# Performance work log

Measured on AMD Instinct MI355X. Metric: run time of the kernel, lower is better.

Reference implementation:

```python
import jax, jax.numpy as jnp
import numpy as np

DIM = 512
N_HEADS = 8
HEAD_DIM = DIM // N_HEADS


def setup_inputs() -> dict:
    key = jax.random.key(0)
    ks = jax.random.split(key, 11)
    B, S = 2, 2048
    s = 1.0 / np.sqrt(DIM)
    return {
        "q": jax.random.normal(ks[0], (B, S, DIM), jnp.float32),
        "k": jax.random.normal(ks[1], (B, S, DIM), jnp.float32),
        "v": jax.random.normal(ks[2], (B, S, DIM), jnp.float32),
        "Wq": jax.random.normal(ks[3], (DIM, DIM), jnp.float32) * s,
        "bq": jnp.zeros((DIM,), jnp.float32),
        "Wk": jax.random.normal(ks[4], (DIM, DIM), jnp.float32) * s,
        "bk": jnp.zeros((DIM,), jnp.float32),
        "Wv": jax.random.normal(ks[5], (DIM, DIM), jnp.float32) * s,
        "bv": jnp.zeros((DIM,), jnp.float32),
        "Wo": jax.random.normal(ks[6], (DIM, DIM), jnp.float32) * s,
        "bo": jnp.zeros((DIM,), jnp.float32),
    }


def reference(q, k, v, Wq, bq, Wk, bk, Wv, bv, Wo, bo):
    B, S, _ = q.shape
    # projections; split into heads: [B, H, S, Dh]
    def proj(x, W, b):
        y = x @ W.T + b
        return y.reshape(B, -1, N_HEADS, HEAD_DIM).transpose(0, 2, 1, 3)

    qh = proj(q, Wq, bq)
    kh = proj(k, Wk, bk)
    vh = proj(v, Wv, bv)
    scores = jnp.einsum("bhsd,bhtd->bhst", qh, kh) / np.sqrt(HEAD_DIM)
    attn = jax.nn.softmax(scores, axis=-1)  # dropout = identity in eval
    ctx = jnp.einsum("bhst,bhtd->bhsd", attn, vh)
    ctx = ctx.transpose(0, 2, 1, 3).reshape(B, S, DIM)
    out = ctx @ Wo.T + bo
    return out, attn
```

## Files before the change

kernel.cpp:

```cpp
#include <hip/hip_runtime.h>
#include <math.h>

#define DIM 512
#define NH 8
#define HD 64
#define SS 2048
#define NB 2

typedef __bf16 bf16;
typedef __attribute__((ext_vector_type(8))) __bf16 bf16x8;
typedef __attribute__((ext_vector_type(4))) __bf16 bf16x4;
typedef __attribute__((ext_vector_type(2))) __bf16 bf16x2;
typedef __attribute__((ext_vector_type(4))) float f32x4;

__device__ inline bf16x8 cvt8(const float* s) {
  bf16x8 o;
#pragma unroll
  for (int i = 0; i < 8; ++i) o[i] = (bf16)s[i];
  return o;
}

__device__ inline void bar_lds_only() {
  asm volatile("s_waitcnt lgkmcnt(0)" ::: "memory");
  __builtin_amdgcn_s_barrier();
}

__global__ __launch_bounds__(256) void qkv_proj_kernel(
    const float* __restrict__ xq, const float* __restrict__ xk, const float* __restrict__ xv,
    const float* __restrict__ Wq, const float* __restrict__ bq,
    const float* __restrict__ Wk, const float* __restrict__ bk,
    const float* __restrict__ Wv, const float* __restrict__ bv,
    bf16* __restrict__ qh, bf16* __restrict__ kh, bf16* __restrict__ vh)
{
  const int which = blockIdx.z;
  const float* A    = (which == 0) ? xq : (which == 1) ? xk : xv;
  const float* W    = (which == 0) ? Wq : (which == 1) ? Wk : Wv;
  const float* bias = (which == 0) ? bq : (which == 1) ? bk : bv;
  bf16* out         = (which == 0) ? qh : (which == 1) ? kh : vh;
  const float oscale = (which == 0) ? 0.125f : 1.0f;

  __shared__ bf16 As[128][72];
  __shared__ bf16 Bs[64][72];

  const int m0 = blockIdx.x * 128;
  const int n0 = blockIdx.y * 64;
  const int tid = threadIdx.x;
  const int w = tid >> 6, l = tid & 63;
  const int l16 = l & 15, lg = l >> 4;
  const int wm = w >> 1, wn = w & 1;

  f32x4 acc[4][2];
#pragma unroll
  for (int mf = 0; mf < 4; ++mf)
#pragma unroll
    for (int nf = 0; nf < 2; ++nf) acc[mf][nf] = (f32x4){0.f, 0.f, 0.f, 0.f};

  for (int k0 = 0; k0 < DIM; k0 += 64) {
    __syncthreads();
    {
      const int r = tid >> 1, hf = (tid & 1) * 32;
      const float* src = &A[(size_t)(m0 + r) * DIM + k0 + hf];
      bf16* dst = &As[r][hf];
#pragma unroll
      for (int i = 0; i < 4; ++i) ((bf16x8*)dst)[i] = cvt8(src + i * 8);
    }
    if (tid < 128) {
      const int r = tid >> 1, hf = (tid & 1) * 32;
      const float* src = &W[(size_t)(n0 + r) * DIM + k0 + hf];
      bf16* dst = &Bs[r][hf];
#pragma unroll
      for (int i = 0; i < 4; ++i) ((bf16x8*)dst)[i] = cvt8(src + i * 8);
    }
    __syncthreads();

#pragma unroll
    for (int kk = 0; kk < 2; ++kk) {
      bf16x8 bfr[2];
      bfr[0] = *(const bf16x8*)&Bs[wn * 32 + l16][kk * 32 + lg * 8];
      bfr[1] = *(const bf16x8*)&Bs[wn * 32 + 16 + l16][kk * 32 + lg * 8];
#pragma unroll
      for (int mf = 0; mf < 4; ++mf) {
        const bf16x8 af = *(const bf16x8*)&As[wm * 64 + mf * 16 + l16][kk * 32 + lg * 8];
        acc[mf][0] = __builtin_amdgcn_mfma_f32_16x16x32_bf16(af, bfr[0], acc[mf][0], 0, 0, 0);
        acc[mf][1] = __builtin_amdgcn_mfma_f32_16x16x32_bf16(af, bfr[1], acc[mf][1], 0, 0, 0);
      }
    }
  }

  const int h = blockIdx.y;
#pragma unroll
  for (int mf = 0; mf < 4; ++mf) {
#pragma unroll
    for (int nf = 0; nf < 2; ++nf) {
      const int d = wn * 32 + nf * 16 + l16;
#pragma unroll
      for (int ri = 0; ri < 4; ++ri) {
        const int row = m0 + wm * 64 + mf * 16 + lg * 4 + ri;
        const int b = row >> 11, s = row & 2047;
        out[((size_t)(b * NH + h) * SS + s) * HD + d] =
            (bf16)((acc[mf][nf][ri] + bias[n0 + d]) * oscale);
      }
    }
  }
}

__global__ __launch_bounds__(256, 8) void sums_kernel(
    const bf16* __restrict__ qh, const bf16* __restrict__ kh,
    float* __restrict__ partial)
{
  __shared__ __align__(16) bf16 Ks[2][64][72];

  const int lin  = blockIdx.x;
  const int work = (lin & 7) * 128 + (lin >> 3);
  const int half = work & 1;
  const int qb   = (work >> 1) & 31;
  const int bh   = work >> 6;
  const int q0   = qb * 64;

  const int tid = threadIdx.x;
  const int w   = tid >> 6;
  const int l   = tid & 63;
  const int l16 = l & 15;
  const int lg  = l >> 4;

  const bf16* qp = qh + (size_t)bh * SS * HD;
  const bf16* kp = kh + ((size_t)bh * SS + half * 1024) * HD;

  const int ks_r = tid >> 2;
  const int ks_c = (tid & 3) * 16;
  const bf16* kstage = &kp[(size_t)ks_r * HD + ks_c];

  const int qrow = q0 + w * 16 + l16;
  const bf16x8 qf0 = *(const bf16x8*)&qp[(size_t)qrow * HD + lg * 8];
  const bf16x8 qf1 = *(const bf16x8*)&qp[(size_t)qrow * HD + 32 + lg * 8];

  {
    ((bf16x8*)&Ks[0][ks_r][ks_c])[0] = ((const bf16x8*)kstage)[0];
    ((bf16x8*)&Ks[0][ks_r][ks_c])[1] = ((const bf16x8*)kstage)[1];
  }
  bar_lds_only();

  float lsum = 0.f;
  int cur = 0;
  for (int tt = 0; tt < 1024; tt += 64) {
    bf16x8 kr0, kr1;
    const bool has_next = (tt + 64) < 1024;
    if (has_next) {
      const bf16* src = kstage + (size_t)(tt + 64) * HD;
      kr0 = ((const bf16x8*)src)[0];
      kr1 = ((const bf16x8*)src)[1];
    }

#pragma unroll
    for (int n = 0; n < 4; ++n) {
      const bf16x8 kf0 = *(const bf16x8*)&Ks[cur][n * 16 + l16][lg * 8];
      const bf16x8 kf1 = *(const bf16x8*)&Ks[cur][n * 16 + l16][32 + lg * 8];
      f32x4 a = {0.f, 0.f, 0.f, 0.f};
      a = __builtin_amdgcn_mfma_f32_16x16x32_bf16(kf0, qf0, a, 0, 0, 0);
      a = __builtin_amdgcn_mfma_f32_16x16x32_bf16(kf1, qf1, a, 0, 0, 0);
#pragma unroll
      for (int reg = 0; reg < 4; ++reg) lsum += __expf(a[reg]);
    }
    if (has_next) {
      ((bf16x8*)&Ks[cur ^ 1][ks_r][ks_c])[0] = kr0;
      ((bf16x8*)&Ks[cur ^ 1][ks_r][ks_c])[1] = kr1;
    }
    bar_lds_only();
    cur ^= 1;
  }

  lsum += __shfl_xor(lsum, 16);
  lsum += __shfl_xor(lsum, 32);
  if (lg == 0) partial[(((size_t)bh * SS) + q0 + w * 16 + l16) * 2 + half] = lsum;
}

__global__ __launch_bounds__(256, 4) void attn_kernel(
    const bf16* __restrict__ qh, const bf16* __restrict__ kh, const bf16* __restrict__ vh,
    const float* __restrict__ partial,
    float* __restrict__ attn, bf16* __restrict__ ctxp)
{
  __shared__ __align__(16) bf16 Ks[64][72];
  __shared__ __align__(16) bf16 Vt[64][72];
  __shared__ __align__(16) bf16 Ps[4][16][80];

  const int lin  = blockIdx.x;
  const int work = (lin & 7) * 256 + (lin >> 3);
  const int tq   = work & 3;
  const int qb   = (work >> 2) & 31;
  const int bh   = work >> 7;
  const int q0   = qb * 64;
  const int t0b  = tq * 512;

  const int tid = threadIdx.x;
  const int w   = tid >> 6;
  const int l   = tid & 63;
  const int l16 = l & 15;
  const int lg  = l >> 4;

  const bf16* qp = qh + (size_t)bh * SS * HD;
  const bf16* kp = kh + (size_t)bh * SS * HD;
  const bf16* vp = vh + (size_t)bh * SS * HD;

  const int ks_r  = tid >> 2;
  const int ks_c  = (tid & 3) * 16;
  const int vs_rc = (tid >> 3) & 31;
  const int vs_dc = tid & 7;

  const bf16* kstage = &kp[(size_t)(t0b + ks_r) * HD + ks_c];
  const bf16* vstage = &vp[(size_t)(t0b + vs_rc * 2) * HD + vs_dc * 8];
  bf16* ks_dst = &Ks[ks_r][ks_c];
  const int vcolbase = (((vs_rc >> 2) ^ vs_dc) << 3) | ((vs_rc & 3) << 1);

  const int qrow = q0 + w * 16 + l16;
  const bf16x8 qf0 = *(const bf16x8*)&qp[(size_t)qrow * HD + lg * 8];
  const bf16x8 qf1 = *(const bf16x8*)&qp[(size_t)qrow * HD + 32 + lg * 8];

  const float inv_l = 1.f / (partial[((size_t)bh * SS + qrow) * 2 + 0] +
                             partial[((size_t)bh * SS + qrow) * 2 + 1]);

  f32x4 accC[4];
#pragma unroll
  for (int dt = 0; dt < 4; ++dt) accC[dt] = (f32x4){0.f, 0.f, 0.f, 0.f};

  float* arow = attn + ((size_t)(bh * SS + qrow)) * SS + t0b;
  char* psbase = (char*)&Ps[w][0][0] + l16 * 160;

  {
    ((bf16x8*)ks_dst)[0] = ((const bf16x8*)kstage)[0];
    ((bf16x8*)ks_dst)[1] = ((const bf16x8*)kstage)[1];
    const bf16x8 v0 = *(const bf16x8*)vstage;
    const bf16x8 v1 = *(const bf16x8*)(vstage + HD);
#pragma unroll
    for (int j = 0; j < 8; ++j) {
      *(bf16x2*)&Vt[vs_dc * 8 + j][vcolbase] = (bf16x2){v0[j], v1[j]};
    }
  }

  for (int tt = 0; tt < 512; tt += 64) {
    bf16x8 kr0, kr1, vr0, vr1;
    const bool has_next = (tt + 64) < 512;
    if (has_next) {
      const bf16* ksrc = kstage + (size_t)(tt + 64) * HD;
      kr0 = ((const bf16x8*)ksrc)[0];
      kr1 = ((const bf16x8*)ksrc)[1];
      const bf16* vsrc = vstage + (size_t)(tt + 64) * HD;
      vr0 = *(const bf16x8*)vsrc;
      vr1 = *(const bf16x8*)(vsrc + HD);
    }
    bar_lds_only();

#pragma unroll
    for (int n = 0; n < 4; ++n) {
      const bf16x8 kf0 = *(const bf16x8*)&Ks[n * 16 + l16][lg * 8];
      const bf16x8 kf1 = *(const bf16x8*)&Ks[n * 16 + l16][32 + lg * 8];
      f32x4 a = {0.f, 0.f, 0.f, 0.f};
      a = __builtin_amdgcn_mfma_f32_16x16x32_bf16(kf0, qf0, a, 0, 0, 0);
      a = __builtin_amdgcn_mfma_f32_16x16x32_bf16(kf1, qf1, a, 0, 0, 0);

      float4 pv;
      bf16x4 p4;
#pragma unroll
      for (int reg = 0; reg < 4; ++reg) {
        const float p = __expf(a[reg]) * inv_l;
        ((float*)&pv)[reg] = p;
        p4[reg] = (bf16)p;
      }
      *(float4*)&arow[tt + n * 16 + lg * 4] = pv;
      *(bf16x4*)(psbase + ((((n << 1) | (lg >> 1)) ^ (l16 & 7)) << 4) + ((lg & 1) << 3)) = p4;
    }

#pragma unroll
    for (int ts = 0; ts < 2; ++ts) {
      const bf16x8 pa = *(const bf16x8*)(psbase + ((((ts << 2) | lg) ^ (l16 & 7)) << 4));
#pragma unroll
      for (int dt = 0; dt < 4; ++dt) {
        const int vcol = (((ts * 4 + lg) ^ ((dt * 2 + (l16 >> 3)) & 7)) << 3);
        const bf16x8 vb = *(const bf16x8*)&Vt[dt * 16 + l16][vcol];
        accC[dt] = __builtin_amdgcn_mfma_f32_16x16x32_bf16(vb, pa, accC[dt], 0, 0, 0);
      }
    }
    bar_lds_only();
    if (has_next) {
      ((bf16x8*)ks_dst)[0] = kr0;
      ((bf16x8*)ks_dst)[1] = kr1;
#pragma unroll
      for (int j = 0; j < 8; ++j) {
        *(bf16x2*)&Vt[vs_dc * 8 + j][vcolbase] = (bf16x2){vr0[j], vr1[j]};
      }
    }
  }

  const int b = bh >> 3, h = bh & 7;
  bf16* crow = ctxp + (size_t)tq * NB * SS * DIM +
               ((size_t)b * SS + qrow) * DIM + h * HD;
#pragma unroll
  for (int dt = 0; dt < 4; ++dt) {
    bf16x4 cb;
#pragma unroll
    for (int reg = 0; reg < 4; ++reg) cb[reg] = (bf16)accC[dt][reg];
    *(bf16x4*)&crow[dt * 16 + lg * 4] = cb;
  }
}

__global__ __launch_bounds__(256) void out_proj_kernel(
    const bf16* __restrict__ ctxp, const float* __restrict__ Wo, const float* __restrict__ bo,
    float* __restrict__ out)
{
  __shared__ bf16 As[128][72];
  __shared__ bf16 Bs[64][72];

  const size_t CH = (size_t)NB * SS * DIM;

  const int m0 = blockIdx.x * 128;
  const int n0 = blockIdx.y * 64;
  const int tid = threadIdx.x;
  const int w = tid >> 6, l = tid & 63;
  const int l16 = l & 15, lg = l >> 4;
  const int wm = w >> 1, wn = w & 1;

  f32x4 acc[4][2];
#pragma unroll
  for (int mf = 0; mf < 4; ++mf)
#pragma unroll
    for (int nf = 0; nf < 2; ++nf) acc[mf][nf] = (f32x4){0.f, 0.f, 0.f, 0.f};

  for (int k0 = 0; k0 < DIM; k0 += 64) {
    __syncthreads();
    {
      const int r = tid >> 1, hf = (tid & 1) * 32;
      const bf16* s0 = &ctxp[(size_t)(m0 + r) * DIM + k0 + hf];
      bf16* dst = &As[r][hf];
#pragma unroll
      for (int i = 0; i < 4; ++i) {
        const bf16x8 a0 = ((const bf16x8*)s0)[i];
        const bf16x8 a1 = ((const bf16x8*)(s0 + CH))[i];
        const bf16x8 a2 = ((const bf16x8*)(s0 + 2 * CH))[i];
        const bf16x8 a3 = ((const bf16x8*)(s0 + 3 * CH))[i];
        bf16x8 o;
#pragma unroll
        for (int j = 0; j < 8; ++j)
          o[j] = (bf16)((float)a0[j] + (float)a1[j] + (float)a2[j] + (float)a3[j]);
        ((bf16x8*)dst)[i] = o;
      }
    }
    if (tid < 128) {
      const int r = tid >> 1, hf = (tid & 1) * 32;
      const float* src = &Wo[(size_t)(n0 + r) * DIM + k0 + hf];
      bf16* dst = &Bs[r][hf];
#pragma unroll
      for (int i = 0; i < 4; ++i) ((bf16x8*)dst)[i] = cvt8(src + i * 8);
    }
    __syncthreads();

#pragma unroll
    for (int kk = 0; kk < 2; ++kk) {
      bf16x8 bfr[2];
      bfr[0] = *(const bf16x8*)&Bs[wn * 32 + l16][kk * 32 + lg * 8];
      bfr[1] = *(const bf16x8*)&Bs[wn * 32 + 16 + l16][kk * 32 + lg * 8];
#pragma unroll
      for (int mf = 0; mf < 4; ++mf) {
        const bf16x8 af = *(const bf16x8*)&As[wm * 64 + mf * 16 + l16][kk * 32 + lg * 8];
        acc[mf][0] = __builtin_amdgcn_mfma_f32_16x16x32_bf16(af, bfr[0], acc[mf][0], 0, 0, 0);
        acc[mf][1] = __builtin_amdgcn_mfma_f32_16x16x32_bf16(af, bfr[1], acc[mf][1], 0, 0, 0);
      }
    }
  }

#pragma unroll
  for (int mf = 0; mf < 4; ++mf) {
#pragma unroll
    for (int nf = 0; nf < 2; ++nf) {
      const int c = n0 + wn * 32 + nf * 16 + l16;
#pragma unroll
      for (int ri = 0; ri < 4; ++ri) {
        const int row = m0 + wm * 64 + mf * 16 + lg * 4 + ri;
        out[(size_t)row * DIM + c] = acc[mf][nf][ri] + bo[c];
      }
    }
  }
}

extern "C" void kernel_launch(void* const* d_in, const int* in_sizes, int n_in,
                              void* d_out, int out_size, void* d_ws, size_t ws_size,
                              hipStream_t stream) {
  const float* q  = (const float*)d_in[0];
  const float* k  = (const float*)d_in[1];
  const float* v  = (const float*)d_in[2];
  const float* Wq = (const float*)d_in[3];
  const float* bq = (const float*)d_in[4];
  const float* Wk = (const float*)d_in[5];
  const float* bk = (const float*)d_in[6];
  const float* Wv = (const float*)d_in[7];
  const float* bv = (const float*)d_in[8];
  const float* Wo = (const float*)d_in[9];
  const float* bo = (const float*)d_in[10];

  float* out0 = (float*)d_out;
  float* attn = out0 + (size_t)NB * SS * DIM;

  const size_t HSZ = (size_t)NB * NH * SS * HD;
  bf16* qh   = (bf16*)d_ws;
  bf16* kh   = qh + HSZ;
  bf16* vh   = kh + HSZ;
  bf16* ctxp = vh + HSZ;
  float* partial = (float*)(ctxp + 4 * (size_t)NB * SS * DIM);

  dim3 g1(NB * SS / 128, DIM / 64, 3);
  qkv_proj_kernel<<<g1, 256, 0, stream>>>(q, k, v, Wq, bq, Wk, bk, Wv, bv, qh, kh, vh);

  dim3 g2a(NB * NH * (SS / 64) * 2);
  sums_kernel<<<g2a, 256, 0, stream>>>(qh, kh, partial);

  dim3 g2(NB * NH * (SS / 64) * 4);
  attn_kernel<<<g2, 256, 0, stream>>>(qh, kh, vh, partial, attn, ctxp);

  dim3 g3(NB * SS / 128, DIM / 64);
  out_proj_kernel<<<g3, 256, 0, stream>>>(ctxp, Wo, bo, out0);
}
```

Before: 150.9 us.

## Write V pre-transposed from projection and read K/V directly from global in attention

```diff
diff --git a/kernel.cpp b/kernel.cpp
--- a/kernel.cpp
+++ b/kernel.cpp
@@ -10,7 +10,6 @@
 typedef __bf16 bf16;
 typedef __attribute__((ext_vector_type(8))) __bf16 bf16x8;
 typedef __attribute__((ext_vector_type(4))) __bf16 bf16x4;
-typedef __attribute__((ext_vector_type(2))) __bf16 bf16x2;
 typedef __attribute__((ext_vector_type(4))) float f32x4;
 
 __device__ inline bf16x8 cvt8(const float* s) {
@@ -25,18 +24,17 @@
   __builtin_amdgcn_s_barrier();
 }
 
-__global__ __launch_bounds__(256) void qkv_proj_kernel(
-    const float* __restrict__ xq, const float* __restrict__ xk, const float* __restrict__ xv,
+__global__ __launch_bounds__(256) void qk_proj_kernel(
+    const float* __restrict__ xq, const float* __restrict__ xk,
     const float* __restrict__ Wq, const float* __restrict__ bq,
     const float* __restrict__ Wk, const float* __restrict__ bk,
-    const float* __restrict__ Wv, const float* __restrict__ bv,
-    bf16* __restrict__ qh, bf16* __restrict__ kh, bf16* __restrict__ vh)
+    bf16* __restrict__ qh, bf16* __restrict__ kh)
 {
   const int which = blockIdx.z;
-  const float* A    = (which == 0) ? xq : (which == 1) ? xk : xv;
-  const float* W    = (which == 0) ? Wq : (which == 1) ? Wk : Wv;
-  const float* bias = (which == 0) ? bq : (which == 1) ? bk : bv;
-  bf16* out         = (which == 0) ? qh : (which == 1) ? kh : vh;
+  const float* A    = (which == 0) ? xq : xk;
+  const float* W    = (which == 0) ? Wq : Wk;
+  const float* bias = (which == 0) ? bq : bk;
+  bf16* out         = (which == 0) ? qh : kh;
   const float oscale = (which == 0) ? 0.125f : 1.0f;
 
   __shared__ bf16 As[128][72];
@@ -99,6 +97,76 @@
         const int b = row >> 11, s = row & 2047;
         out[((size_t)(b * NH + h) * SS + s) * HD + d] =
             (bf16)((acc[mf][nf][ri] + bias[n0 + d]) * oscale);
+      }
+    }
+  }
+}
+
+__global__ __launch_bounds__(256) void vprojT_kernel(
+    const float* __restrict__ xv, const float* __restrict__ Wv, const float* __restrict__ bv,
+    bf16* __restrict__ vT)
+{
+  __shared__ bf16 Ws[64][72];
+  __shared__ bf16 Xs[128][72];
+
+  const int n0 = blockIdx.x * 128;
+  const int h  = blockIdx.y;
+  const int tid = threadIdx.x;
+  const int w = tid >> 6, l = tid & 63;
+  const int l16 = l & 15, lg = l >> 4;
+  const int wm = w >> 1, wn = w & 1;
+
+  f32x4 acc[2][4];
+#pragma unroll
+  for (int mf = 0; mf < 2; ++mf)
+#pragma unroll
+    for (int nf = 0; nf < 4; ++nf) acc[mf][nf] = (f32x4){0.f, 0.f, 0.f, 0.f};
+
+  for (int k0 = 0; k0 < DIM; k0 += 64) {
+    __syncthreads();
+    {
+      const int r = tid >> 1, hf = (tid & 1) * 32;
+      const float* src = &xv[(size_t)(n0 + r) * DIM + k0 + hf];
+      bf16* dst = &Xs[r][hf];
+#pragma unroll
+      for (int i = 0; i < 4; ++i) ((bf16x8*)dst)[i] = cvt8(src + i * 8);
+    }
+    if (tid < 128) {
+      const int r = tid >> 1, hf = (tid & 1) * 32;
+      const float* src = &Wv[(size_t)(h * 64 + r) * DIM + k0 + hf];
+      bf16* dst = &Ws[r][hf];
+#pragma unroll
+      for (int i = 0; i < 4; ++i) ((bf16x8*)dst)[i] = cvt8(src + i * 8);
+    }
+    __syncthreads();
+
+#pragma unroll
+    for (int kk = 0; kk < 2; ++kk) {
+      bf16x8 af[2];
+#pragma unroll
+      for (int mf = 0; mf < 2; ++mf)
+        af[mf] = *(const bf16x8*)&Ws[wm * 32 + mf * 16 + l16][kk * 32 + lg * 8];
+#pragma unroll
+      for (int nf = 0; nf < 4; ++nf) {
+        const bf16x8 bf = *(const bf16x8*)&Xs[wn * 64 + nf * 16 + l16][kk * 32 + lg * 8];
+#pragma unroll
+        for (int mf = 0; mf < 2; ++mf)
+          acc[mf][nf] = __builtin_amdgcn_mfma_f32_16x16x32_bf16(af[mf], bf, acc[mf][nf], 0, 0, 0);
+      }
+    }
+  }
+
+  const int b = n0 >> 11, s0 = n0 & 2047;
+#pragma unroll
+  for (int mf = 0; mf < 2; ++mf) {
+#pragma unroll
+    for (int nf = 0; nf < 4; ++nf) {
+#pragma unroll
+      for (int ri = 0; ri < 4; ++ri) {
+        const int dloc = wm * 32 + mf * 16 + lg * 4 + ri;
+        const int sloc = wn * 64 + nf * 16 + l16;
+        vT[((size_t)(b * NH + h) * HD + dloc) * SS + s0 + sloc] =
+            (bf16)(acc[mf][nf][ri] + bv[h * 64 + dloc]);
       }
     }
   }
@@ -175,21 +243,19 @@
 }
 
 __global__ __launch_bounds__(256, 4) void attn_kernel(
-    const bf16* __restrict__ qh, const bf16* __restrict__ kh, const bf16* __restrict__ vh,
+    const bf16* __restrict__ qh, const bf16* __restrict__ kh, const bf16* __restrict__ vT,
     const float* __restrict__ partial,
     float* __restrict__ attn, bf16* __restrict__ ctxp)
 {
-  __shared__ __align__(16) bf16 Ks[64][72];
-  __shared__ __align__(16) bf16 Vt[64][72];
   __shared__ __align__(16) bf16 Ps[4][16][80];
 
   const int lin  = blockIdx.x;
-  const int work = (lin & 7) * 256 + (lin >> 3);
-  const int tq   = work & 3;
-  const int qb   = (work >> 2) & 31;
-  const int bh   = work >> 7;
+  const int work = (lin & 7) * 128 + (lin >> 3);
+  const int half = work & 1;
+  const int qb   = (work >> 1) & 31;
+  const int bh   = work >> 6;
   const int q0   = qb * 64;
-  const int t0b  = tq * 512;
+  const int t0b  = half * 1024;
 
   const int tid = threadIdx.x;
   const int w   = tid >> 6;
@@ -197,19 +263,9 @@
   const int l16 = l & 15;
   const int lg  = l >> 4;
 
-  const bf16* qp = qh + (size_t)bh * SS * HD;
-  const bf16* kp = kh + (size_t)bh * SS * HD;
-  const bf16* vp = vh + (size_t)bh * SS * HD;
-
-  const int ks_r  = tid >> 2;
-  const int ks_c  = (tid & 3) * 16;
-  const int vs_rc = (tid >> 3) & 31;
-  const int vs_dc = tid & 7;
-
-  const bf16* kstage = &kp[(size_t)(t0b + ks_r) * HD + ks_c];
-  const bf16* vstage = &vp[(size_t)(t0b + vs_rc * 2) * HD + vs_dc * 8];
-  bf16* ks_dst = &Ks[ks_r][ks_c];
-  const int vcolbase = (((vs_rc >> 2) ^ vs_dc) << 3) | ((vs_rc & 3) << 1);
+  const bf16* qp  = qh + (size_t)bh * SS * HD;
+  const bf16* kp  = kh + ((size_t)bh * SS + t0b) * HD;
+  const bf16* vtp = vT + (size_t)bh * HD * SS + t0b;
 
   const int qrow = q0 + w * 16 + l16;
   const bf16x8 qf0 = *(const bf16x8*)&qp[(size_t)qrow * HD + lg * 8];
@@ -225,34 +281,12 @@
   float* arow = attn + ((size_t)(bh * SS + qrow)) * SS + t0b;
   char* psbase = (char*)&Ps[w][0][0] + l16 * 160;
 
-  {
-    ((bf16x8*)ks_dst)[0] = ((const bf16x8*)kstage)[0];
-    ((bf16x8*)ks_dst)[1] = ((const bf16x8*)kstage)[1];
-    const bf16x8 v0 = *(const bf16x8*)vstage;
-    const bf16x8 v1 = *(const bf16x8*)(vstage + HD);
-#pragma unroll
-    for (int j = 0; j < 8; ++j) {
-      *(bf16x2*)&Vt[vs_dc * 8 + j][vcolbase] = (bf16x2){v0[j], v1[j]};
-    }
-  }
-
-  for (int tt = 0; tt < 512; tt += 64) {
-    bf16x8 kr0, kr1, vr0, vr1;
-    const bool has_next = (tt + 64) < 512;
-    if (has_next) {
-      const bf16* ksrc = kstage + (size_t)(tt + 64) * HD;
-      kr0 = ((const bf16x8*)ksrc)[0];
-      kr1 = ((const bf16x8*)ksrc)[1];
-      const bf16* vsrc = vstage + (size_t)(tt + 64) * HD;
-      vr0 = *(const bf16x8*)vsrc;
-      vr1 = *(const bf16x8*)(vsrc + HD);
-    }
-    bar_lds_only();
-
+  for (int tt = 0; tt < 1024; tt += 64) {
 #pragma unroll
     for (int n = 0; n < 4; ++n) {
-      const bf16x8 kf0 = *(const bf16x8*)&Ks[n * 16 + l16][lg * 8];
-      const bf16x8 kf1 = *(const bf16x8*)&Ks[n * 16 + l16][32 + lg * 8];
+      const bf16* krow = &kp[(size_t)(tt + n * 16 + l16) * HD + lg * 8];
+      const bf16x8 kf0 = *(const bf16x8*)krow;
+      const bf16x8 kf1 = *(const bf16x8*)(krow + 32);
       f32x4 a = {0.f, 0.f, 0.f, 0.f};
       a = __builtin_amdgcn_mfma_f32_16x16x32_bf16(kf0, qf0, a, 0, 0, 0);
       a = __builtin_amdgcn_mfma_f32_16x16x32_bf16(kf1, qf1, a, 0, 0, 0);
@@ -274,24 +308,15 @@
       const bf16x8 pa = *(const bf16x8*)(psbase + ((((ts << 2) | lg) ^ (l16 & 7)) << 4));
 #pragma unroll
       for (int dt = 0; dt < 4; ++dt) {
-        const int vcol = (((ts * 4 + lg) ^ ((dt * 2 + (l16 >> 3)) & 7)) << 3);
-        const bf16x8 vb = *(const bf16x8*)&Vt[dt * 16 + l16][vcol];
+        const bf16x8 vb =
+            *(const bf16x8*)&vtp[(size_t)(dt * 16 + l16) * SS + tt + ts * 32 + lg * 8];
         accC[dt] = __builtin_amdgcn_mfma_f32_16x16x32_bf16(vb, pa, accC[dt], 0, 0, 0);
       }
     }
-    bar_lds_only();
-    if (has_next) {
-      ((bf16x8*)ks_dst)[0] = kr0;
-      ((bf16x8*)ks_dst)[1] = kr1;
-#pragma unroll
-      for (int j = 0; j < 8; ++j) {
-        *(bf16x2*)&Vt[vs_dc * 8 + j][vcolbase] = (bf16x2){vr0[j], vr1[j]};
-      }
-    }
   }
 
   const int b = bh >> 3, h = bh & 7;
-  bf16* crow = ctxp + (size_t)tq * NB * SS * DIM +
+  bf16* crow = ctxp + (size_t)half * NB * SS * DIM +
                ((size_t)b * SS + qrow) * DIM + h * HD;
 #pragma unroll
   for (int dt = 0; dt < 4; ++dt) {
@@ -334,12 +359,9 @@
       for (int i = 0; i < 4; ++i) {
         const bf16x8 a0 = ((const bf16x8*)s0)[i];
         const bf16x8 a1 = ((const bf16x8*)(s0 + CH))[i];
-        const bf16x8 a2 = ((const bf16x8*)(s0 + 2 * CH))[i];
-        const bf16x8 a3 = ((const bf16x8*)(s0 + 3 * CH))[i];
         bf16x8 o;
 #pragma unroll
-        for (int j = 0; j < 8; ++j)
-          o[j] = (bf16)((float)a0[j] + (float)a1[j] + (float)a2[j] + (float)a3[j]);
+        for (int j = 0; j < 8; ++j) o[j] = (bf16)((float)a0[j] + (float)a1[j]);
         ((bf16x8*)dst)[i] = o;
       }
     }
@@ -401,18 +423,21 @@
   const size_t HSZ = (size_t)NB * NH * SS * HD;
   bf16* qh   = (bf16*)d_ws;
   bf16* kh   = qh + HSZ;
-  bf16* vh   = kh + HSZ;
-  bf16* ctxp = vh + HSZ;
-  float* partial = (float*)(ctxp + 4 * (size_t)NB * SS * DIM);
-
-  dim3 g1(NB * SS / 128, DIM / 64, 3);
-  qkv_proj_kernel<<<g1, 256, 0, stream>>>(q, k, v, Wq, bq, Wk, bk, Wv, bv, qh, kh, vh);
+  bf16* vT   = kh + HSZ;
+  bf16* ctxp = vT + HSZ;
+  float* partial = (float*)(ctxp + 2 * (size_t)NB * SS * DIM);
+
+  dim3 g1(NB * SS / 128, DIM / 64, 2);
+  qk_proj_kernel<<<g1, 256, 0, stream>>>(q, k, Wq, bq, Wk, bk, qh, kh);
+
+  dim3 g1b(NB * SS / 128, NH);
+  vprojT_kernel<<<g1b, 256, 0, stream>>>(v, Wv, bv, vT);
 
   dim3 g2a(NB * NH * (SS / 64) * 2);
   sums_kernel<<<g2a, 256, 0, stream>>>(qh, kh, partial);
 
-  dim3 g2(NB * NH * (SS / 64) * 4);
-  attn_kernel<<<g2, 256, 0, stream>>>(qh, kh, vh, partial, attn, ctxp);
+  dim3 g2(NB * NH * (SS / 64) * 2);
+  attn_kernel<<<g2, 256, 0, stream>>>(qh, kh, vT, partial, attn, ctxp);
 
   dim3 g3(NB * SS / 128, DIM / 64);
   out_proj_kernel<<<g3, 256, 0, stream>>>(ctxp, Wo, bo, out0);
```

After: 223.9 us. 48.3% more time.
